# Optimization experiments

Measured on AMD Instinct MI355X. Metric: run time of the kernel, lower is better.

## Reference

```python
import jax, jax.numpy as jnp
import numpy as np

B, C, T, H, F, KS = 8, 512, 1024, 8, 2048, 3
K = C // H            # head channels = 64
ROPE_D = K // 2       # RoPE rotates half the head channels = 32
EPS = 1e-4


def setup_inputs() -> dict:
    key = jax.random.key(0)
    ks = jax.random.split(key, 12)
    s = 1.0 / np.sqrt(C)
    sf = 1.0 / np.sqrt(F)
    return {
        "x": jax.random.normal(ks[0], (B, C, T), jnp.float32),
        "x_mask": jnp.ones((B, 1, T), jnp.float32),
        "attn_mask": jnp.ones((B, 1, T, T), jnp.float32),
        "wq": jax.random.normal(ks[1], (C, C), jnp.float32) * s,
        "bq": jnp.zeros((C,), jnp.float32),
        "wk": jax.random.normal(ks[2], (C, C), jnp.float32) * s,
        "bk": jnp.zeros((C,), jnp.float32),
        "wv": jax.random.normal(ks[3], (C, C), jnp.float32) * s,
        "bv": jnp.zeros((C,), jnp.float32),
        "wo": jax.random.normal(ks[4], (C, C), jnp.float32) * s,
        "bo": jnp.zeros((C,), jnp.float32),
        "w1": jax.random.normal(ks[5], (F, C, KS), jnp.float32) * s,
        "b1": jnp.zeros((F,), jnp.float32),
        "w2": jax.random.normal(ks[6], (C, F, KS), jnp.float32) * sf,
        "b2": jnp.zeros((C,), jnp.float32),
        "g1": jnp.ones((C,), jnp.float32),
        "be1": jnp.zeros((C,), jnp.float32),
        "g2": jnp.ones((C,), jnp.float32),
        "be2": jnp.zeros((C,), jnp.float32),
    }


def _rope(x):
    # x: (B, H, T, K); rotate first ROPE_D channels, pass the rest through.
    t = x.shape[2]
    theta = 1.0 / (10000.0 ** (jnp.arange(0, ROPE_D, 2, dtype=jnp.float32) / ROPE_D))
    idx = jnp.arange(t, dtype=jnp.float32)[:, None] * theta[None, :]  # (T, d/2)
    idx2 = jnp.concatenate([idx, idx], axis=-1)                       # (T, d)
    cos, sin = jnp.cos(idx2), jnp.sin(idx2)                           # broadcast over B,H
    xr, xp = x[..., :ROPE_D], x[..., ROPE_D:]
    h = ROPE_D // 2
    neg = jnp.concatenate([-xr[..., h:], xr[..., :h]], axis=-1)
    return jnp.concatenate([xr * cos + neg * sin, xp], axis=-1)


def _ln(x, gamma, beta):
    # channel-wise LayerNorm over dim 1 of (B, C, T), eps=1e-4
    mean = jnp.mean(x, axis=1, keepdims=True)
    var = jnp.mean((x - mean) ** 2, axis=1, keepdims=True)
    xn = (x - mean) * jax.lax.rsqrt(var + EPS)
    return xn * gamma[None, :, None] + beta[None, :, None]


def _conv1d(x, w, b):
    # x: (B, Cin, T), w: (Cout, Cin, KS), 'same' padding (KS//2)
    y = jax.lax.conv_general_dilated(
        x, w, window_strides=(1,), padding=[(KS // 2, KS // 2)],
        dimension_numbers=("NCH", "OIH", "NCH"))
    return y + b[None, :, None]


def _forward(x, x_mask, attn_mask, wq, bq, wk, bk, wv, bv, wo, bo,
             w1, b1, w2, b2, g1, be1, g2, be2):
    x = x * x_mask
    # 1x1 conv projections == channel matmuls
    q = jnp.einsum("oc,bct->bot", wq, x) + bq[None, :, None]
    k = jnp.einsum("oc,bct->bot", wk, x) + bk[None, :, None]
    v = jnp.einsum("oc,bct->bot", wv, x) + bv[None, :, None]
    # (B, C, T) -> (B, H, T, K)
    def heads(a):
        return a.reshape(B, H, K, T).transpose(0, 1, 3, 2)
    q, k, v = heads(q), heads(k), heads(v)
    q = _rope(q)
    k = _rope(k)
    scores = jnp.einsum("bhtk,bhsk->bhts", q, k) / jnp.sqrt(jnp.float32(K))
    scores = jnp.where(attn_mask == 0, jnp.float32(-10000.0), scores)
    p = jax.nn.softmax(scores, axis=-1)
    o = jnp.einsum("bhts,bhsk->bhtk", p, v)              # (B,H,T,K)
    o = o.transpose(0, 1, 3, 2).reshape(B, C, T)
    y = jnp.einsum("oc,bct->bot", wo, o) + bo[None, :, None]
    x = _ln(x + y, g1, be1)
    # conv FFN
    h1 = jax.nn.relu(_conv1d(x * x_mask, w1, b1))
    y = _conv1d(h1 * x_mask, w2, b2) * x_mask
    x = _ln(x + y, g2, be2)
    return x


def reference(x, x_mask, attn_mask, wq, bq, wk, bk, wv, bv, wo, bo,
              w1, b1, w2, b2, g1, be1, g2, be2):
    return _forward(x, x_mask, attn_mask, wq, bq, wk, bk, wv, bv, wo, bo,
                    w1, b1, w2, b2, g1, be1, g2, be2)
```

## Files before the change

kernel.cpp:

```cpp
#include <hip/hip_runtime.h>

typedef unsigned short u16;
typedef __attribute__((ext_vector_type(4))) float floatx4;
typedef __attribute__((ext_vector_type(8))) __bf16 bf16x8;
typedef __attribute__((ext_vector_type(4))) unsigned short ushort4v;
typedef __attribute__((ext_vector_type(8))) unsigned short ushort8v;

#define DI __device__ __forceinline__


DI u16 f2bf(float f) {
  union { float f; unsigned u; } v; v.f = f;
  unsigned r = v.u + 0x7fffu + ((v.u >> 16) & 1u);
  return (u16)(r >> 16);
}
DI float bf2f(u16 h) {
  union { unsigned u; float f; } v; v.u = ((unsigned)h) << 16;
  return v.f;
}

#define GLDS(g, l) __builtin_amdgcn_global_load_lds( \
    (const __attribute__((address_space(1))) unsigned int*)(g), \
    (__attribute__((address_space(3))) unsigned int*)(l), 16, 0, 0)

__global__ __launch_bounds__(256, 2) void k_fattn(
    const u16* __restrict__ qb, const u16* __restrict__ kb,
    const u16* __restrict__ vb, const unsigned* __restrict__ mb,
    u16* __restrict__ oT)
{
  __shared__ __align__(16) u16 Ps[4][32 * 64];
  const int tid  = threadIdx.x;
  const int wave = tid >> 6, lane = tid & 63;
  const int lr = lane & 15, kg = lane >> 4;
  const int qt = blockIdx.x, bh = blockIdx.y;
  const int bb = bh >> 3, hh = bh & 7;
  const int wq0 = qt * 128 + wave * 32;
  const float L2E = 1.44269504f;

  const u16* Qp = qb + (size_t)bh * 65536;
  const u16* Kp = kb + (size_t)bh * 65536;
  const u16* Vp = vb + (size_t)bh * 65536;
  u16* Pw = &Ps[wave][0];

  bf16x8 qf[2][2];
#pragma unroll
  for (int i = 0; i < 2; ++i)
#pragma unroll
    for (int h = 0; h < 2; ++h)
      qf[i][h] = *(const bf16x8*)&Qp[(wq0 + i * 16 + lr) * 64 + h * 32 + kg * 8];

  float l_b[2] = {0.f, 0.f};
  floatx4 o_acc[2][4];
#pragma unroll
  for (int i = 0; i < 2; ++i)
#pragma unroll
    for (int j = 0; j < 4; ++j) o_acc[i][j] = (floatx4){0.f, 0.f, 0.f, 0.f};

  bf16x8 kf[4][2], vf[4][2];
#pragma unroll
  for (int a = 0; a < 4; ++a)
#pragma unroll
    for (int h = 0; h < 2; ++h)
      kf[a][h] = *(const bf16x8*)&Kp[(a * 16 + lr) * 64 + h * 32 + kg * 8];

  for (int it = 0; it < 16; ++it) {
    const int s0 = it * 64;
    unsigned mw[2][2];
#pragma unroll
    for (int b = 0; b < 2; ++b) {
      const size_t rw = ((size_t)bb << 15) + ((size_t)(wq0 + b * 16 + lr) << 5) + (s0 >> 5);
      mw[b][0] = mb[rw]; mw[b][1] = mb[rw + 1];
    }
    floatx4 sT[4][2];
    __builtin_amdgcn_s_setprio(1);
#pragma unroll
    for (int a = 0; a < 4; ++a) {
      sT[a][0] = (floatx4){0.f, 0.f, 0.f, 0.f};
      sT[a][1] = (floatx4){0.f, 0.f, 0.f, 0.f};
#pragma unroll
      for (int b = 0; b < 2; ++b)
#pragma unroll
        for (int h = 0; h < 2; ++h)
          sT[a][b] = __builtin_amdgcn_mfma_f32_16x16x32_bf16(kf[a][h], qf[b][h], sT[a][b], 0, 0, 0);
    }
    __builtin_amdgcn_s_setprio(0);
#pragma unroll
    for (int a = 0; a < 4; ++a)
#pragma unroll
      for (int h = 0; h < 2; ++h)
        vf[a][h] = *(const bf16x8*)&Vp[(a * 16 + lr) * 1024 + s0 + h * 32 + kg * 8];
    if (it < 15) {
      const int sn = s0 + 64;
#pragma unroll
      for (int a = 0; a < 4; ++a)
#pragma unroll
        for (int h = 0; h < 2; ++h)
          kf[a][h] = *(const bf16x8*)&Kp[(sn + a * 16 + lr) * 64 + h * 32 + kg * 8];
    }
#pragma unroll
    for (int b = 0; b < 2; ++b) {
      float sum = 0.f;
#pragma unroll
      for (int a = 0; a < 4; ++a)
#pragma unroll
        for (int r = 0; r < 4; ++r) {
          const int sl = a * 16 + kg * 4 + r;
          float sv = sT[a][b][r] * 0.125f;
          const unsigned wsel = (sl & 32) ? mw[b][1] : mw[b][0];
          if (!((wsel >> (sl & 31)) & 1u)) sv = -10000.f;
          const float p = exp2f(sv * L2E);
          sT[a][b][r] = p;
          sum += p;
        }
      sum += __shfl_xor(sum, 16);
      sum += __shfl_xor(sum, 32);
      l_b[b] += sum;
#pragma unroll
      for (int a = 0; a < 4; ++a) {
        ushort4v pk;
#pragma unroll
        for (int r = 0; r < 4; ++r) {
          __bf16 hv = (__bf16)sT[a][b][r];
          pk[r] = *(u16*)&hv;
        }
        const int sl0 = a * 16 + kg * 4;
        *(ushort4v*)&Pw[(b * 16 + lr) * 64 + (sl0 ^ ((lr & 7) << 3))] = pk;
      }
    }
    asm volatile("s_waitcnt lgkmcnt(0)" ::: "memory");
    __builtin_amdgcn_sched_barrier(0);
    bf16x8 pa[2][2];
#pragma unroll
    for (int i = 0; i < 2; ++i)
#pragma unroll
      for (int h = 0; h < 2; ++h)
        pa[i][h] = *(const bf16x8*)&Pw[(i * 16 + lr) * 64 + (((h * 4 + kg) ^ (lr & 7)) << 3)];
    __builtin_amdgcn_s_setprio(1);
#pragma unroll
    for (int jd = 0; jd < 4; ++jd)
#pragma unroll
      for (int i = 0; i < 2; ++i)
#pragma unroll
        for (int h = 0; h < 2; ++h)
          o_acc[i][jd] = __builtin_amdgcn_mfma_f32_16x16x32_bf16(pa[i][h], vf[jd][h], o_acc[i][jd], 0, 0, 0);
    __builtin_amdgcn_s_setprio(0);
  }
  float linv[2][4];
#pragma unroll
  for (int i = 0; i < 2; ++i)
#pragma unroll
    for (int r = 0; r < 4; ++r) linv[i][r] = 1.f / __shfl(l_b[i], kg * 4 + r);
#pragma unroll
  for (int i = 0; i < 2; ++i)
#pragma unroll
    for (int jd = 0; jd < 4; ++jd)
#pragma unroll
      for (int r = 0; r < 4; ++r) {
        const int t = wq0 + i * 16 + kg * 4 + r;
        const int c = hh * 64 + jd * 16 + lr;
        oT[((size_t)bb * 1024 + t) * 512 + c] = f2bf(o_acc[i][jd][r] * linv[i][r]);
      }
}

template<int MODE, int BN, int TAPK>
__global__ __launch_bounds__(256) void k_cgemm(
    const u16* __restrict__ A, int lda,
    const u16* __restrict__ Bsrc, int ldb,
    int K,
    u16* __restrict__ o0, u16* __restrict__ o1, u16* __restrict__ o2,
    const float* __restrict__ bias,
    const float* __restrict__ ctab, const float* __restrict__ stab,
    const float* __restrict__ msk)
{
  constexpr int BM = 128;
  constexpr int FN = BN / 32;
  __shared__ __align__(16) u16 As[2 * BM * 32];
  __shared__ __align__(16) u16 Bs[2 * BN * 32];

  const int tid  = threadIdx.x;
  const int wave = tid >> 6, lane = tid & 63;
  const int wm = wave >> 1, wn = wave & 1;
  const int lr = lane & 15, kg = lane >> 4;

  const int nwg = gridDim.x * gridDim.y;
  const int h0  = blockIdx.y * gridDim.x + blockIdx.x;
  const int cpx = nwg >> 3;
  const int tl  = (h0 & 7) * cpx + (h0 >> 3);
  const int bx  = tl % gridDim.x;
  const int by  = tl / gridDim.x;

  const int m0 = bx * BM, n0 = by * BN;
  const int koff = blockIdx.z * K;

  floatx4 acc[4][FN];
#pragma unroll
  for (int i = 0; i < 4; ++i)
#pragma unroll
    for (int j = 0; j < FN; ++j) acc[i][j] = (floatx4){0.f, 0.f, 0.f, 0.f};

  const int csw = (kg ^ ((lr >> 1) & 3)) * 8;

  for (int k0 = 0; k0 < K; k0 += 64) {
#pragma unroll
    for (int h = 0; h < 2; ++h) {
      const int kglob = koff + k0 + h * 32;
#pragma unroll
      for (int ch = 0; ch < BM / 64; ++ch) {
        const int idx = ch * 256 + tid;
        const int row = idx >> 2;
        const int kk = (((idx & 3) ^ ((row >> 1) & 3)) << 3);
        GLDS(A + (size_t)(m0 + row) * lda + (kglob + kk),
             &As[h * BM * 32 + idx * 8]);
      }
#pragma unroll
      for (int ch = 0; ch < BN / 64; ++ch) {
        const int idx = ch * 256 + tid;
        const int row = idx >> 2;
        const int kk = (((idx & 3) ^ ((row >> 1) & 3)) << 3);
        const int bt = n0 + row;
        const u16* src;
        if constexpr (TAPK == 0) {
          src = Bsrc + (size_t)bt * ldb + (kglob + kk);
        } else {
          const int tap = kglob / TAPK, off2 = kglob - tap * TAPK;
          const int b = bt >> 10, t = bt & 1023;
          src = Bsrc + ((size_t)(b * 1026 + t + tap)) * TAPK + off2 + kk;
        }
        GLDS(src, &Bs[h * BN * 32 + idx * 8]);
      }
    }
    __syncthreads();
    bf16x8 af[2][4], bfr[2][FN];
#pragma unroll
    for (int h = 0; h < 2; ++h) {
#pragma unroll
      for (int i = 0; i < 4; ++i)
        af[h][i] = *(const bf16x8*)&As[(h * BM + wm * 64 + i * 16 + lr) * 32 + csw];
#pragma unroll
      for (int j = 0; j < FN; ++j)
        bfr[h][j] = *(const bf16x8*)&Bs[(h * BN + wn * (BN / 2) + j * 16 + lr) * 32 + csw];
    }
#pragma unroll
    for (int h = 0; h < 2; ++h)
#pragma unroll
      for (int i = 0; i < 4; ++i)
#pragma unroll
        for (int j = 0; j < FN; ++j)
          acc[i][j] = __builtin_amdgcn_mfma_f32_16x16x32_bf16(af[h][i], bfr[h][j], acc[i][j], 0, 0, 0);
    __syncthreads();
  }

  const int wrow0 = m0 + wm * 64;
  const int col0  = n0 + wn * (BN / 2);

  if constexpr (MODE == 0) {
    float v[4][FN][4];
#pragma unroll
    for (int i = 0; i < 4; ++i)
#pragma unroll
      for (int j = 0; j < FN; ++j)
#pragma unroll
        for (int r = 0; r < 4; ++r)
          v[i][j][r] = acc[i][j][r] + bias[wrow0 + i * 16 + kg * 4 + r];
    const int sec = wrow0 >> 9;
    const int hh  = (wrow0 & 511) >> 6;
    if (sec < 2) {
#pragma unroll
      for (int j = 0; j < FN; ++j) {
        const int t = (col0 + j * 16 + lr) & 1023;
#pragma unroll
        for (int r = 0; r < 4; ++r) {
          const int a = kg * 4 + r;
          const float cv = ctab[t * 16 + a], sv = stab[t * 16 + a];
          const float a0 = v[0][j][r], a1 = v[1][j][r];
          v[0][j][r] = a0 * cv - a1 * sv;
          v[1][j][r] = a1 * cv + a0 * sv;
        }
      }
      u16* dst = (sec == 0) ? o0 : o1;
#pragma unroll
      for (int i = 0; i < 4; ++i)
#pragma unroll
        for (int j = 0; j < FN; ++j) {
          const int bt = col0 + j * 16 + lr;
          const int b = bt >> 10, t = bt & 1023;
          ushort4v pk;
#pragma unroll
          for (int r = 0; r < 4; ++r) pk[r] = f2bf(v[i][j][r]);
          *(ushort4v*)&dst[(((size_t)b * 8 + hh) * 1024 + t) * 64 + i * 16 + kg * 4] = pk;
        }
    } else {
#pragma unroll
      for (int i = 0; i < 4; ++i)
#pragma unroll
        for (int j = 0; j < FN; ++j) {
          const int bt = col0 + j * 16 + lr;
          const int b = bt >> 10, t = bt & 1023;
#pragma unroll
          for (int r = 0; r < 4; ++r) {
            const int dk = i * 16 + kg * 4 + r;
            o2[(((size_t)b * 8 + hh) * 64 + dk) * 1024 + t] = f2bf(v[i][j][r]);
          }
        }
    }
  } else if constexpr (MODE == 3) {
#pragma unroll
    for (int i = 0; i < 4; ++i)
#pragma unroll
      for (int j = 0; j < FN; ++j) {
        const int bt = col0 + j * 16 + lr;
        const int c0 = wrow0 + i * 16 + kg * 4;
        ushort4v pk;
#pragma unroll
        for (int r = 0; r < 4; ++r) pk[r] = f2bf(acc[i][j][r] + bias[c0 + r]);
        *(ushort4v*)&o0[(size_t)bt * 512 + c0] = pk;
      }
  } else if constexpr (MODE == 4) {
#pragma unroll
    for (int i = 0; i < 4; ++i) {
      const int r0 = wrow0 + i * 16 + kg * 4;
#pragma unroll
      for (int j = 0; j < FN; ++j) {
        const int bt = col0 + j * 16 + lr;
        const int b = bt >> 10, t = bt & 1023;
        const float mv = msk[(size_t)b * 1024 + t];
        ushort4v pk;
#pragma unroll
        for (int r = 0; r < 4; ++r)
          pk[r] = f2bf(fmaxf(acc[i][j][r] + bias[r0 + r], 0.f) * mv);
        *(ushort4v*)&o0[((size_t)(b * 1026 + t + 1)) * 2048 + r0] = pk;
      }
    }
  } else {
    u16* dst = (blockIdx.z == 0) ? o0 : o1;
#pragma unroll
    for (int i = 0; i < 4; ++i)
#pragma unroll
      for (int j = 0; j < FN; ++j) {
        const int bt = col0 + j * 16 + lr;
        const int b = bt >> 10, t = bt & 1023;
        const int c0 = wrow0 + i * 16 + kg * 4;
        const float mv = msk[(size_t)b * 1024 + t];
        ushort4v pk;
#pragma unroll
        for (int r = 0; r < 4; ++r) {
          const float bv = (blockIdx.z == 0) ? bias[c0 + r] : 0.f;
          pk[r] = f2bf((acc[i][j][r] + bv) * mv);
        }
        *(ushort4v*)&dst[(size_t)bt * 512 + c0] = pk;
      }
  }
}

__global__ __launch_bounds__(256) void k_cvt(const float* __restrict__ in, u16* __restrict__ out, int n) {
  int i = blockIdx.x * 256 + threadIdx.x;
  if (i < n) out[i] = f2bf(in[i]);
}

__global__ __launch_bounds__(256) void k_repack_w1(const float* __restrict__ in, u16* __restrict__ out) {
  int i = blockIdx.x * 256 + threadIdx.x;
  int f = i / 1536, rem = i % 1536;
  int kk = rem >> 9, c = rem & 511;
  out[i] = f2bf(in[f * 1536 + c * 3 + kk]);
}

__global__ __launch_bounds__(256) void k_repack_w2(const float* __restrict__ in, u16* __restrict__ out) {
  int i = blockIdx.x * 256 + threadIdx.x;
  int c = i / 6144, rem = i % 6144;
  int kk = rem >> 11, f = rem & 2047;
  out[i] = f2bf(in[c * 6144 + f * 3 + kk]);
}

__global__ __launch_bounds__(256) void k_bias_concat(const float* __restrict__ bq, const float* __restrict__ bk,
                                                     const float* __restrict__ bv, float* __restrict__ out) {
  int i = blockIdx.x * 256 + threadIdx.x;
  if (i < 512) out[i] = bq[i];
  else if (i < 1024) out[i] = bk[i - 512];
  else if (i < 1536) out[i] = bv[i - 1024];
}

__global__ __launch_bounds__(256) void k_rope_tables(float* __restrict__ ct, float* __restrict__ st) {
  int i = blockIdx.x * 256 + threadIdx.x;
  int t = i >> 4, a = i & 15;
  float theta = powf(10000.f, -(float)a / 16.f);
  float ang = (float)t * theta;
  ct[i] = cosf(ang);
  st[i] = sinf(ang);
}

__global__ __launch_bounds__(256) void k_maskpack(const float* __restrict__ am, unsigned* __restrict__ mb) {
  int i = blockIdx.x * 256 + threadIdx.x;
  const float* src = am + (size_t)i * 32;
  unsigned w = 0;
#pragma unroll
  for (int q = 0; q < 32; ++q) w |= (src[q] != 0.f) ? (1u << q) : 0u;
  mb[i] = w;
}

__global__ __launch_bounds__(256) void k_zrows(u16* __restrict__ p, int R) {
  const int b = blockIdx.x >> 1;
  const size_t row = (blockIdx.x & 1) ? 1025 : 0;
  u16* r = p + ((size_t)b * 1026 + row) * R;
  for (int i = threadIdx.x; i < R; i += 256) r[i] = 0;
}

__global__ __launch_bounds__(256) void k_tcvt(const float* __restrict__ in, u16* __restrict__ out,
                                              const float* __restrict__ msk, int R, int TT) {
  __shared__ u16 tile[64][65];
  const int b = blockIdx.z;
  const int r0 = blockIdx.x * 64, t0 = blockIdx.y * 64;
  const int tx = threadIdx.x & 63, ty = threadIdx.x >> 6;
  const float mv = msk ? msk[(size_t)b * TT + t0 + tx] : 1.f;
  const float* ib = in + (size_t)b * R * TT;
#pragma unroll
  for (int rr = ty; rr < 64; rr += 4)
    tile[rr][tx] = f2bf(ib[(size_t)(r0 + rr) * TT + t0 + tx] * mv);
  __syncthreads();
  u16* ob = out + (size_t)b * TT * R;
#pragma unroll
  for (int tt = ty; tt < 64; tt += 4)
    ob[(size_t)(t0 + tt) * R + r0 + tx] = tile[tx][tt];
}

__global__ __launch_bounds__(256) void k_ln1(
    const u16* __restrict__ xbT, const u16* __restrict__ y1T,
    const float* __restrict__ xm, const float* __restrict__ g,
    const float* __restrict__ be, u16* __restrict__ x2T, u16* __restrict__ x2p)
{
  const int lane = threadIdx.x & 63, wv = threadIdx.x >> 6;
  const int row = blockIdx.x * 4 + wv;
  const int b = row >> 10, t = row & 1023;
  const size_t base = (size_t)row * 512 + lane * 8;
  ushort8v ux = *(const ushort8v*)&xbT[base];
  ushort8v uy = *(const ushort8v*)&y1T[base];
  float v[8];
  float sum = 0.f, ss = 0.f;
#pragma unroll
  for (int q = 0; q < 8; ++q) {
    v[q] = bf2f(ux[q]) + bf2f(uy[q]);
    sum += v[q]; ss += v[q] * v[q];
  }
#pragma unroll
  for (int o = 32; o; o >>= 1) { sum += __shfl_xor(sum, o); ss += __shfl_xor(ss, o); }
  const float mean = sum * (1.f / 512.f);
  const float var  = ss * (1.f / 512.f) - mean * mean;
  const float rs   = rsqrtf(var + 1e-4f);
  const float m    = xm[(size_t)b * 1024 + t];
  ushort8v on, om;
#pragma unroll
  for (int q = 0; q < 8; ++q) {
    const int c = lane * 8 + q;
    const float nv = (v[q] - mean) * rs * g[c] + be[c];
    on[q] = f2bf(nv);
    om[q] = f2bf(nv * m);
  }
  *(ushort8v*)&x2T[base] = on;
  *(ushort8v*)&x2p[((size_t)(b * 1026 + t + 1)) * 512 + lane * 8] = om;
}

__global__ __launch_bounds__(256) void k_ln2_stats(
    const u16* __restrict__ x2T, const u16* __restrict__ y2a,
    const u16* __restrict__ y2b, float2* __restrict__ mr)
{
  const int lane = threadIdx.x & 63, wv = threadIdx.x >> 6;
  const int row = blockIdx.x * 4 + wv;
  const size_t base = (size_t)row * 512 + lane * 8;
  ushort8v u0 = *(const ushort8v*)&x2T[base];
  ushort8v u1 = *(const ushort8v*)&y2a[base];
  ushort8v u2 = *(const ushort8v*)&y2b[base];
  float sum = 0.f, ss = 0.f;
#pragma unroll
  for (int q = 0; q < 8; ++q) {
    const float v = bf2f(u0[q]) + bf2f(u1[q]) + bf2f(u2[q]);
    sum += v; ss += v * v;
  }
#pragma unroll
  for (int o = 32; o; o >>= 1) { sum += __shfl_xor(sum, o); ss += __shfl_xor(ss, o); }
  if (lane == 0) {
    const float mean = sum * (1.f / 512.f);
    const float var  = ss * (1.f / 512.f) - mean * mean;
    mr[row] = (float2){mean, rsqrtf(var + 1e-4f)};
  }
}

__global__ __launch_bounds__(256) void k_ln2_write(
    const u16* __restrict__ x2T, const u16* __restrict__ y2a,
    const u16* __restrict__ y2b, const float2* __restrict__ mr,
    const float* __restrict__ g, const float* __restrict__ be,
    float* __restrict__ out)
{
  __shared__ float tile[64][65];
  const int cc0 = blockIdx.x * 64, t0 = blockIdx.y * 64, b = blockIdx.z;
  const int tid = threadIdx.x;
  const int c4 = (tid & 15) * 4;
  const int tr = tid >> 4;
  float g4[4], b4[4];
#pragma unroll
  for (int q = 0; q < 4; ++q) { g4[q] = g[cc0 + c4 + q]; b4[q] = be[cc0 + c4 + q]; }
#pragma unroll
  for (int it = 0; it < 4; ++it) {
    const int tt = tr + it * 16;
    const int row = b * 1024 + t0 + tt;
    const size_t base = (size_t)row * 512 + cc0 + c4;
    ushort4v u0 = *(const ushort4v*)&x2T[base];
    ushort4v u1 = *(const ushort4v*)&y2a[base];
    ushort4v u2 = *(const ushort4v*)&y2b[base];
    const float2 s = mr[row];
#pragma unroll
    for (int q = 0; q < 4; ++q) {
      const float v = bf2f(u0[q]) + bf2f(u1[q]) + bf2f(u2[q]);
      tile[tt][c4 + q] = (v - s.x) * s.y * g4[q] + b4[q];
    }
  }
  __syncthreads();
  const int tx = tid & 63, cg = tid >> 6;
#pragma unroll
  for (int c = cg; c < 64; c += 4)
    out[((size_t)b * 512 + cc0 + c) * 1024 + t0 + tx] = tile[tx][c];
}

extern "C" void kernel_launch(void* const* d_in, const int* in_sizes, int n_in,
                              void* d_out, int out_size, void* d_ws, size_t ws_size,
                              hipStream_t stream) {
  (void)in_sizes; (void)n_in; (void)out_size; (void)ws_size;
  const float* x   = (const float*)d_in[0];
  const float* xm  = (const float*)d_in[1];
  const float* am  = (const float*)d_in[2];
  const float* wq  = (const float*)d_in[3];
  const float* bq  = (const float*)d_in[4];
  const float* wk  = (const float*)d_in[5];
  const float* bk  = (const float*)d_in[6];
  const float* wv  = (const float*)d_in[7];
  const float* bv  = (const float*)d_in[8];
  const float* wo  = (const float*)d_in[9];
  const float* bo  = (const float*)d_in[10];
  const float* w1  = (const float*)d_in[11];
  const float* b1  = (const float*)d_in[12];
  const float* w2  = (const float*)d_in[13];
  const float* b2  = (const float*)d_in[14];
  const float* g1  = (const float*)d_in[15];
  const float* be1 = (const float*)d_in[16];
  const float* g2  = (const float*)d_in[17];
  const float* be2 = (const float*)d_in[18];
  float* out = (float*)d_out;

  char* ws = (char*)d_ws;
  size_t off = 0;
  auto alloc = [&](size_t bytes) { char* p = ws + off; off += (bytes + 255) & ~(size_t)255; return p; };

  u16*   wqkv = (u16*)  alloc((size_t)1536 * 512 * 2);
  u16*   wob  = (u16*)  alloc((size_t)512 * 512 * 2);
  u16*   w1p  = (u16*)  alloc((size_t)2048 * 1536 * 2);
  u16*   w2p  = (u16*)  alloc((size_t)512 * 6144 * 2);
  float* bqkv = (float*)alloc(1536 * 4);
  float* ctab = (float*)alloc(1024 * 16 * 4);
  float* stab = (float*)alloc(1024 * 16 * 4);
  unsigned* mbits = (unsigned*)alloc((size_t)8 * 1024 * 32 * 4);
  float2* mr  = (float2*)alloc((size_t)8192 * 8);
  u16*   x2T  = (u16*)  alloc((size_t)8 * 1024 * 512 * 2);
  u16*   x2p  = (u16*)  alloc((size_t)8 * 1026 * 512 * 2);
  u16*   h1p  = (u16*)  alloc((size_t)8 * 1026 * 2048 * 2);
  u16*   y1T  = (u16*)  alloc((size_t)8 * 1024 * 512 * 2);
  u16*   xbT  = (u16*)  alloc((size_t)8 * 1024 * 512 * 2);
  u16*   oT   = (u16*)  alloc((size_t)8 * 1024 * 512 * 2);
  u16*   qkv3 = (u16*)  alloc((size_t)3 * 8 * 8 * 1024 * 64 * 2);

  u16* qb   = qkv3;
  u16* kb   = qkv3 + (size_t)8 * 8 * 1024 * 64;
  u16* vb   = kb   + (size_t)8 * 8 * 1024 * 64;
  u16* y2aT = y1T;
  u16* y2bT = oT;

  dim3 blk(256);

  k_cvt<<<dim3(1024), blk, 0, stream>>>(wq, wqkv, 512 * 512);
  k_cvt<<<dim3(1024), blk, 0, stream>>>(wk, wqkv + 512 * 512, 512 * 512);
  k_cvt<<<dim3(1024), blk, 0, stream>>>(wv, wqkv + 2 * 512 * 512, 512 * 512);
  k_cvt<<<dim3(1024), blk, 0, stream>>>(wo, wob, 512 * 512);
  k_repack_w1<<<dim3(12288), blk, 0, stream>>>(w1, w1p);
  k_repack_w2<<<dim3(12288), blk, 0, stream>>>(w2, w2p);
  k_bias_concat<<<dim3(6), blk, 0, stream>>>(bq, bk, bv, bqkv);
  k_rope_tables<<<dim3(64), blk, 0, stream>>>(ctab, stab);
  k_maskpack<<<dim3(1024), blk, 0, stream>>>(am, mbits);
  k_zrows<<<dim3(16), blk, 0, stream>>>(x2p, 512);
  k_zrows<<<dim3(16), blk, 0, stream>>>(h1p, 2048);

  k_tcvt<<<dim3(8, 16, 8), blk, 0, stream>>>(x, xbT, xm, 512, 1024);

  k_cgemm<0, 128, 0><<<dim3(12, 64), blk, 0, stream>>>(
      wqkv, 512, xbT, 512, 512, qb, kb, vb, bqkv, ctab, stab, nullptr);

  k_fattn<<<dim3(8, 64), blk, 0, stream>>>(qb, kb, vb, mbits, oT);

  k_cgemm<3, 64, 0><<<dim3(4, 128), blk, 0, stream>>>(
      wob, 512, oT, 512, 512, y1T, nullptr, nullptr, bo, nullptr, nullptr, nullptr);

  k_ln1<<<dim3(2048), blk, 0, stream>>>(xbT, y1T, xm, g1, be1, x2T, x2p);

  k_cgemm<4, 128, 512><<<dim3(16, 64), blk, 0, stream>>>(
      w1p, 1536, x2p, 0, 1536, h1p, nullptr, nullptr, b1, nullptr, nullptr, xm);
  k_cgemm<5, 64, 2048><<<dim3(4, 128, 2), blk, 0, stream>>>(
      w2p, 6144, h1p, 0, 3072, y2aT, y2bT, nullptr, b2, nullptr, nullptr, xm);

  k_ln2_stats<<<dim3(2048), blk, 0, stream>>>(x2T, y2aT, y2bT, mr);
  k_ln2_write<<<dim3(8, 16, 8), blk, 0, stream>>>(x2T, y2aT, y2bT, mr, g2, be2, out);
}
```

Baseline: 320.6 us.

## Merge prep kernels into one launch and split conv2 GEMM four ways over K

Eleven small preprocessing kernels (weight casts and repacks, mask packing, RoPE tables, bias concat, zeroing of padding rows) become one block-indexed kernel, removing launch gaps between them. The second conv GEMM moves from a 2-way to a 4-way split over its reduction dimension with wider N tiles (128). The four partial results go to a new contiguous buffer, and both LayerNorm-2 kernels sum all four partials. This trades more partial-sum writes and reads, plus four bf16 roundings, for better GEMM occupancy and fewer launches.

After: 311.3 us. -2.9%, faster.

```diff
diff --git a/kernel.cpp b/kernel.cpp
--- a/kernel.cpp
+++ b/kernel.cpp
@@ -332,7 +332,8 @@
       }
     }
   } else {
-    u16* dst = (blockIdx.z == 0) ? o0 : o1;
+    u16* dst = o0 + (size_t)blockIdx.z * 8 * 1024 * 512;
+    const bool z0 = (blockIdx.z == 0);
 #pragma unroll
     for (int i = 0; i < 4; ++i)
 #pragma unroll
@@ -344,7 +345,7 @@
         ushort4v pk;
 #pragma unroll
         for (int r = 0; r < 4; ++r) {
-          const float bv = (blockIdx.z == 0) ? bias[c0 + r] : 0.f;
+          const float bv = z0 ? bias[c0 + r] : 0.f;
           pk[r] = f2bf((acc[i][j][r] + bv) * mv);
         }
         *(ushort4v*)&dst[(size_t)bt * 512 + c0] = pk;
@@ -352,56 +353,66 @@
   }
 }
 
-__global__ __launch_bounds__(256) void k_cvt(const float* __restrict__ in, u16* __restrict__ out, int n) {
-  int i = blockIdx.x * 256 + threadIdx.x;
-  if (i < n) out[i] = f2bf(in[i]);
-}
-
-__global__ __launch_bounds__(256) void k_repack_w1(const float* __restrict__ in, u16* __restrict__ out) {
-  int i = blockIdx.x * 256 + threadIdx.x;
-  int f = i / 1536, rem = i % 1536;
-  int kk = rem >> 9, c = rem & 511;
-  out[i] = f2bf(in[f * 1536 + c * 3 + kk]);
-}
-
-__global__ __launch_bounds__(256) void k_repack_w2(const float* __restrict__ in, u16* __restrict__ out) {
-  int i = blockIdx.x * 256 + threadIdx.x;
-  int c = i / 6144, rem = i % 6144;
-  int kk = rem >> 11, f = rem & 2047;
-  out[i] = f2bf(in[c * 6144 + f * 3 + kk]);
-}
-
-__global__ __launch_bounds__(256) void k_bias_concat(const float* __restrict__ bq, const float* __restrict__ bk,
-                                                     const float* __restrict__ bv, float* __restrict__ out) {
-  int i = blockIdx.x * 256 + threadIdx.x;
-  if (i < 512) out[i] = bq[i];
-  else if (i < 1024) out[i] = bk[i - 512];
-  else if (i < 1536) out[i] = bv[i - 1024];
-}
-
-__global__ __launch_bounds__(256) void k_rope_tables(float* __restrict__ ct, float* __restrict__ st) {
-  int i = blockIdx.x * 256 + threadIdx.x;
-  int t = i >> 4, a = i & 15;
-  float theta = powf(10000.f, -(float)a / 16.f);
-  float ang = (float)t * theta;
-  ct[i] = cosf(ang);
-  st[i] = sinf(ang);
-}
-
-__global__ __launch_bounds__(256) void k_maskpack(const float* __restrict__ am, unsigned* __restrict__ mb) {
-  int i = blockIdx.x * 256 + threadIdx.x;
-  const float* src = am + (size_t)i * 32;
-  unsigned w = 0;
-#pragma unroll
-  for (int q = 0; q < 32; ++q) w |= (src[q] != 0.f) ? (1u << q) : 0u;
-  mb[i] = w;
-}
-
-__global__ __launch_bounds__(256) void k_zrows(u16* __restrict__ p, int R) {
-  const int b = blockIdx.x >> 1;
-  const size_t row = (blockIdx.x & 1) ? 1025 : 0;
-  u16* r = p + ((size_t)b * 1026 + row) * R;
-  for (int i = threadIdx.x; i < R; i += 256) r[i] = 0;
+__global__ __launch_bounds__(256) void k_prep(
+    const float* __restrict__ wq, const float* __restrict__ wk,
+    const float* __restrict__ wv, const float* __restrict__ wo,
+    const float* __restrict__ w1, const float* __restrict__ w2,
+    const float* __restrict__ bq, const float* __restrict__ bk,
+    const float* __restrict__ bv, const float* __restrict__ am,
+    u16* __restrict__ wqkv, u16* __restrict__ wob,
+    u16* __restrict__ w1p, u16* __restrict__ w2p,
+    float* __restrict__ bqkv, float* __restrict__ ctab, float* __restrict__ stab,
+    unsigned* __restrict__ mbits, u16* __restrict__ x2p, u16* __restrict__ h1p)
+{
+  const int bid = blockIdx.x;
+  if (bid < 4096) {
+    const int seg = bid >> 10;
+    const int i = (bid & 1023) * 256 + threadIdx.x;
+    const float* src = (seg == 0) ? wq : (seg == 1) ? wk : (seg == 2) ? wv : wo;
+    u16* dst = (seg < 3) ? (wqkv + (size_t)seg * 512 * 512) : wob;
+    dst[i] = f2bf(src[i]);
+  } else if (bid < 16384) {
+    const int i = (bid - 4096) * 256 + threadIdx.x;
+    const int f = i / 1536, rem = i % 1536;
+    const int kk = rem >> 9, c = rem & 511;
+    w1p[i] = f2bf(w1[f * 1536 + c * 3 + kk]);
+  } else if (bid < 28672) {
+    const int i = (bid - 16384) * 256 + threadIdx.x;
+    const int c = i / 6144, rem = i % 6144;
+    const int kk = rem >> 11, f = rem & 2047;
+    w2p[i] = f2bf(w2[c * 6144 + f * 3 + kk]);
+  } else if (bid < 29696) {
+    const int i = (bid - 28672) * 256 + threadIdx.x;
+    const float* src = am + (size_t)i * 32;
+    unsigned w = 0;
+#pragma unroll
+    for (int q = 0; q < 32; ++q) w |= (src[q] != 0.f) ? (1u << q) : 0u;
+    mbits[i] = w;
+  } else if (bid < 29760) {
+    const int i = (bid - 29696) * 256 + threadIdx.x;
+    const int t = i >> 4, a = i & 15;
+    const float theta = powf(10000.f, -(float)a / 16.f);
+    const float ang = (float)t * theta;
+    ctab[i] = cosf(ang);
+    stab[i] = sinf(ang);
+  } else if (bid == 29760) {
+    for (int i = threadIdx.x; i < 1536; i += 256)
+      bqkv[i] = (i < 512) ? bq[i] : (i < 1024) ? bk[i - 512] : bv[i - 1024];
+  } else {
+    int zb = bid - 29761;
+    if (zb < 16) {
+      const int b = zb >> 1;
+      const size_t row = (zb & 1) ? 1025 : 0;
+      u16* r = x2p + ((size_t)b * 1026 + row) * 512;
+      for (int i = threadIdx.x; i < 512; i += 256) r[i] = 0;
+    } else {
+      zb -= 16;
+      const int b = zb >> 1;
+      const size_t row = (zb & 1) ? 1025 : 0;
+      u16* r = h1p + ((size_t)b * 1026 + row) * 2048;
+      for (int i = threadIdx.x; i < 2048; i += 256) r[i] = 0;
+    }
+  }
 }
 
 __global__ __launch_bounds__(256) void k_tcvt(const float* __restrict__ in, u16* __restrict__ out,
@@ -459,19 +470,22 @@
 }
 
 __global__ __launch_bounds__(256) void k_ln2_stats(
-    const u16* __restrict__ x2T, const u16* __restrict__ y2a,
-    const u16* __restrict__ y2b, float2* __restrict__ mr)
+    const u16* __restrict__ x2T, const u16* __restrict__ c2p,
+    float2* __restrict__ mr)
 {
+  constexpr size_t S = (size_t)8 * 1024 * 512;
   const int lane = threadIdx.x & 63, wv = threadIdx.x >> 6;
   const int row = blockIdx.x * 4 + wv;
   const size_t base = (size_t)row * 512 + lane * 8;
   ushort8v u0 = *(const ushort8v*)&x2T[base];
-  ushort8v u1 = *(const ushort8v*)&y2a[base];
-  ushort8v u2 = *(const ushort8v*)&y2b[base];
+  ushort8v u1 = *(const ushort8v*)&c2p[base];
+  ushort8v u2 = *(const ushort8v*)&c2p[S + base];
+  ushort8v u3 = *(const ushort8v*)&c2p[2 * S + base];
+  ushort8v u4 = *(const ushort8v*)&c2p[3 * S + base];
   float sum = 0.f, ss = 0.f;
 #pragma unroll
   for (int q = 0; q < 8; ++q) {
-    const float v = bf2f(u0[q]) + bf2f(u1[q]) + bf2f(u2[q]);
+    const float v = bf2f(u0[q]) + bf2f(u1[q]) + bf2f(u2[q]) + bf2f(u3[q]) + bf2f(u4[q]);
     sum += v; ss += v * v;
   }
 #pragma unroll
@@ -484,11 +498,12 @@
 }
 
 __global__ __launch_bounds__(256) void k_ln2_write(
-    const u16* __restrict__ x2T, const u16* __restrict__ y2a,
-    const u16* __restrict__ y2b, const float2* __restrict__ mr,
+    const u16* __restrict__ x2T, const u16* __restrict__ c2p,
+    const float2* __restrict__ mr,
     const float* __restrict__ g, const float* __restrict__ be,
     float* __restrict__ out)
 {
+  constexpr size_t S = (size_t)8 * 1024 * 512;
   __shared__ float tile[64][65];
   const int cc0 = blockIdx.x * 64, t0 = blockIdx.y * 64, b = blockIdx.z;
   const int tid = threadIdx.x;
@@ -503,12 +518,14 @@
     const int row = b * 1024 + t0 + tt;
     const size_t base = (size_t)row * 512 + cc0 + c4;
     ushort4v u0 = *(const ushort4v*)&x2T[base];
-    ushort4v u1 = *(const ushort4v*)&y2a[base];
-    ushort4v u2 = *(const ushort4v*)&y2b[base];
+    ushort4v u1 = *(const ushort4v*)&c2p[base];
+    ushort4v u2 = *(const ushort4v*)&c2p[S + base];
+    ushort4v u3 = *(const ushort4v*)&c2p[2 * S + base];
+    ushort4v u4 = *(const ushort4v*)&c2p[3 * S + base];
     const float2 s = mr[row];
 #pragma unroll
     for (int q = 0; q < 4; ++q) {
-      const float v = bf2f(u0[q]) + bf2f(u1[q]) + bf2f(u2[q]);
+      const float v = bf2f(u0[q]) + bf2f(u1[q]) + bf2f(u2[q]) + bf2f(u3[q]) + bf2f(u4[q]);
       tile[tt][c4 + q] = (v - s.x) * s.y * g4[q] + b4[q];
     }
   }
@@ -564,26 +581,17 @@
   u16*   xbT  = (u16*)  alloc((size_t)8 * 1024 * 512 * 2);
   u16*   oT   = (u16*)  alloc((size_t)8 * 1024 * 512 * 2);
   u16*   qkv3 = (u16*)  alloc((size_t)3 * 8 * 8 * 1024 * 64 * 2);
-
-  u16* qb   = qkv3;
-  u16* kb   = qkv3 + (size_t)8 * 8 * 1024 * 64;
-  u16* vb   = kb   + (size_t)8 * 8 * 1024 * 64;
-  u16* y2aT = y1T;
-  u16* y2bT = oT;
+  u16*   c2p  = (u16*)  alloc((size_t)4 * 8 * 1024 * 512 * 2);
+
+  u16* qb = qkv3;
+  u16* kb = qkv3 + (size_t)8 * 8 * 1024 * 64;
+  u16* vb = kb   + (size_t)8 * 8 * 1024 * 64;
 
   dim3 blk(256);
 
-  k_cvt<<<dim3(1024), blk, 0, stream>>>(wq, wqkv, 512 * 512);
-  k_cvt<<<dim3(1024), blk, 0, stream>>>(wk, wqkv + 512 * 512, 512 * 512);
-  k_cvt<<<dim3(1024), blk, 0, stream>>>(wv, wqkv + 2 * 512 * 512, 512 * 512);
-  k_cvt<<<dim3(1024), blk, 0, stream>>>(wo, wob, 512 * 512);
-  k_repack_w1<<<dim3(12288), blk, 0, stream>>>(w1, w1p);
-  k_repack_w2<<<dim3(12288), blk, 0, stream>>>(w2, w2p);
-  k_bias_concat<<<dim3(6), blk, 0, stream>>>(bq, bk, bv, bqkv);
-  k_rope_tables<<<dim3(64), blk, 0, stream>>>(ctab, stab);
-  k_maskpack<<<dim3(1024), blk, 0, stream>>>(am, mbits);
-  k_zrows<<<dim3(16), blk, 0, stream>>>(x2p, 512);
-  k_zrows<<<dim3(16), blk, 0, stream>>>(h1p, 2048);
+  k_prep<<<dim3(29793), blk, 0, stream>>>(
+      wq, wk, wv, wo, w1, w2, bq, bk, bv, am,
+      wqkv, wob, w1p, w2p, bqkv, ctab, stab, mbits, x2p, h1p);
 
   k_tcvt<<<dim3(8, 16, 8), blk, 0, stream>>>(x, xbT, xm, 512, 1024);
 
@@ -599,9 +607,9 @@
 
   k_cgemm<4, 128, 512><<<dim3(16, 64), blk, 0, stream>>>(
       w1p, 1536, x2p, 0, 1536, h1p, nullptr, nullptr, b1, nullptr, nullptr, xm);
-  k_cgemm<5, 64, 2048><<<dim3(4, 128, 2), blk, 0, stream>>>(
-      w2p, 6144, h1p, 0, 3072, y2aT, y2bT, nullptr, b2, nullptr, nullptr, xm);
-
-  k_ln2_stats<<<dim3(2048), blk, 0, stream>>>(x2T, y2aT, y2bT, mr);
-  k_ln2_write<<<dim3(8, 16, 8), blk, 0, stream>>>(x2T, y2aT, y2bT, mr, g2, be2, out);
-}
+  k_cgemm<5, 128, 2048><<<dim3(4, 64, 4), blk, 0, stream>>>(
+      w2p, 6144, h1p, 0, 1536, c2p, nullptr, nullptr, b2, nullptr, nullptr, xm);
+
+  k_ln2_stats<<<dim3(2048), blk, 0, stream>>>(x2T, c2p, mr);
+  k_ln2_write<<<dim3(8, 16, 8), blk, 0, stream>>>(x2T, c2p, mr, g2, be2, out);
+}
```
